# Kernel optimization log

Measured on AMD Instinct MI355X. Metric: run time of the kernel, lower is better.

The kernel has to match this reference:

```python
import jax, jax.numpy as jnp
import numpy as np

NUM_EMBEDDINGS = 1024
EMBEDDING_DIM = 256
COMMITMENT_COST = 0.25


def setup_inputs() -> dict:
    key = jax.random.key(0)
    k_z, k_e = jax.random.split(key)
    z = jax.random.normal(k_z, (16, EMBEDDING_DIM, 4096), dtype=jnp.float32)
    # nn.Embedding init: uniform(-1/K, 1/K)
    emb = jax.random.uniform(
        k_e, (NUM_EMBEDDINGS, EMBEDDING_DIM), dtype=jnp.float32,
        minval=-1.0 / NUM_EMBEDDINGS, maxval=1.0 / NUM_EMBEDDINGS)
    return {"z": z, "emb": emb}


def reference(z, emb):
    # z: [B, D, T] -> [B, T, D]
    zt = jnp.transpose(z, (0, 2, 1))
    B, T, D = zt.shape
    flat = zt.reshape(-1, D)  # [N, D]
    dists = (jnp.sum(flat * flat, axis=1, keepdims=True)
             + jnp.sum(emb * emb, axis=1)
             - 2.0 * jnp.matmul(flat, emb.T))
    idx = jnp.argmin(dists, axis=1)          # [N]
    quantized = emb[idx].reshape(B, T, D)    # gather + reshape
    e_latent_loss = jnp.mean((jax.lax.stop_gradient(quantized) - zt) ** 2)
    q_latent_loss = jnp.mean((quantized - jax.lax.stop_gradient(zt)) ** 2)
    loss = q_latent_loss + COMMITMENT_COST * e_latent_loss
    # straight-through estimator
    quantized_st = zt + jax.lax.stop_gradient(quantized - zt)
    return jnp.transpose(quantized_st, (0, 2, 1)), loss
```

## Files before the change

kernel.cpp:

```cpp
#include <hip/hip_runtime.h>
#include <stdint.h>

#define B_   16
#define D_   256
#define T_   4096
#define K_   1024
#define N_   (B_ * T_)
#define BM   64

typedef __attribute__((ext_vector_type(4))) float floatx4;
typedef __attribute__((ext_vector_type(2))) float floatx2;
typedef __attribute__((ext_vector_type(2))) long longx2;

__global__ __launch_bounds__(256) void emb_prep(const float* __restrict__ emb,
                                                uint32_t* __restrict__ embf8,
                                                float* __restrict__ esqh,
                                                float* __restrict__ lossp) {
    int w = threadIdx.x >> 6, lane = threadIdx.x & 63;
    int k = blockIdx.x * 4 + w;
    float4 v = ((const float4*)emb)[k * 64 + lane];
    float a0 = v.x * 1024.f, a1 = v.y * 1024.f, a2 = v.z * 1024.f, a3 = v.w * 1024.f;
    int p = __builtin_amdgcn_cvt_pk_fp8_f32(a0, a1, 0, false);
    p = __builtin_amdgcn_cvt_pk_fp8_f32(a2, a3, p, true);
    int kk = lane >> 3, quad = (lane >> 1) & 3;
    int widx = (k >> 4) * 1024 + (kk >> 1) * 256 + (quad * 16 + (k & 15)) * 4
             + (kk & 1) * 2 + (lane & 1);
    embf8[widx] = (uint32_t)p;
    float ss = a0 * a0 + a1 * a1 + a2 * a2 + a3 * a3;
    #pragma unroll
    for (int off = 32; off; off >>= 1) ss += __shfl_xor(ss, off, 64);
    if (lane == 0) esqh[k] = ss * (0.5f / 1024.f);
    if (blockIdx.x == 0 && threadIdx.x == 0) *lossp = 0.f;
}

__global__ __launch_bounds__(256, 4) void vq_main(const float* __restrict__ z,
                                                  const uint32_t* __restrict__ embf8,
                                                  const float* __restrict__ esqh,
                                                  float* __restrict__ out0,
                                                  float* __restrict__ lossp) {
    __shared__ __align__(16) unsigned char xs[BM * 256];
    __shared__ float wvals[4][BM];
    __shared__ int   pidx[BM];
    __shared__ float zred[4];

    int tid  = threadIdx.x;
    int lane = tid & 63, w = tid >> 6;
    int ml   = lane & 15, quad = lane >> 4;
    int ph   = w >> 1, ch = w & 1;
    int blk  = blockIdx.x;
    int b    = blk >> 6;
    int t0   = (blk & 63) * BM;
    const float* zb = z + (size_t)b * (D_ * T_) + t0;

    float zsq = 0.f;
    {
        int t = lane, hf = (t >> 4) & 1;
        #pragma unroll 2
        for (int j = 0; j < 8; ++j) {
            int dgrp = w + 4 * j;
            int d0 = dgrp * 8;
            float f0 = zb[(d0 + 0) * T_ + t];
            float f1 = zb[(d0 + 1) * T_ + t];
            float f2 = zb[(d0 + 2) * T_ + t];
            float f3 = zb[(d0 + 3) * T_ + t];
            float f4 = zb[(d0 + 4) * T_ + t];
            float f5 = zb[(d0 + 5) * T_ + t];
            float f6 = zb[(d0 + 6) * T_ + t];
            float f7 = zb[(d0 + 7) * T_ + t];
            zsq += f0*f0 + f1*f1 + f2*f2 + f3*f3 + f4*f4 + f5*f5 + f6*f6 + f7*f7;
            uint32_t p0 = (uint32_t)__builtin_amdgcn_cvt_pk_fp8_f32(-f0, -f1, 0, false);
            p0 = (uint32_t)__builtin_amdgcn_cvt_pk_fp8_f32(-f2, -f3, (int)p0, true);
            uint32_t p1 = (uint32_t)__builtin_amdgcn_cvt_pk_fp8_f32(-f4, -f5, 0, false);
            p1 = (uint32_t)__builtin_amdgcn_cvt_pk_fp8_f32(-f6, -f7, (int)p1, true);
            int c = dgrp >> 1, h = dgrp & 1;
            *(uint2*)&xs[t * 256 + ((c ^ (t & 15)) << 4) + ((h ^ hf) << 3)] =
                make_uint2(p0, p1);
        }
    }

    int ct0 = ch * 32;
    const char* ebL = (const char*)embf8 + (size_t)ct0 * 4096 + (size_t)lane * 16;
    longx2 qqA[4], qqB[4];
    float ehA, ehB;
    #pragma unroll
    for (int i = 0; i < 4; ++i)
        qqA[i] = *(const longx2*)(ebL + i * 1024);
    ehA = esqh[ct0 * 16 + ml];

    __syncthreads();

    long afr[2][8];
    #pragma unroll
    for (int ss = 0; ss < 2; ++ss) {
        int s = 2 * ph + ss;
        int pnt = s * 16 + ml;
        #pragma unroll
        for (int kk = 0; kk < 8; ++kk) {
            int c = 2 * kk + (quad >> 1), h = quad & 1;
            afr[ss][kk] = *(const long*)&xs[pnt * 256 + ((c ^ ml) << 4) + ((h ^ (s & 1)) << 3)];
        }
    }

    float bv[2][4];
    #pragma unroll
    for (int ss = 0; ss < 2; ++ss)
        #pragma unroll
        for (int i = 0; i < 4; ++i) bv[ss][i] = 1e30f;

    const floatx4 zv = {0.f, 0.f, 0.f, 0.f};
    const unsigned hi_mask = 0xFFFFFC00u;

#define VQ_PREFETCH(QQ, EH, J)                                                  \
    {                                                                           \
        const char* p_ = ebL + (size_t)(J) * 4096;                              \
        _Pragma("unroll")                                                       \
        for (int i = 0; i < 4; ++i)                                             \
            QQ[i] = *(const longx2*)(p_ + i * 1024);                            \
        EH = esqh[(ct0 + (J)) * 16 + ml];                                       \
    }

#define VQ_STEP(QQ, EH, J)                                                      \
    {                                                                           \
        floatx4 ehv = {EH, EH, EH, EH};                                         \
        floatx4 lo0, lo1, hi0, hi1;                                             \
        lo0 = __builtin_amdgcn_mfma_f32_16x16x32_fp8_fp8(afr[0][0], QQ[0][0], ehv, 0, 0, 0); \
        lo1 = __builtin_amdgcn_mfma_f32_16x16x32_fp8_fp8(afr[1][0], QQ[0][0], ehv, 0, 0, 0); \
        hi0 = __builtin_amdgcn_mfma_f32_16x16x32_fp8_fp8(afr[0][4], QQ[2][0], zv,  0, 0, 0); \
        hi1 = __builtin_amdgcn_mfma_f32_16x16x32_fp8_fp8(afr[1][4], QQ[2][0], zv,  0, 0, 0); \
        lo0 = __builtin_amdgcn_mfma_f32_16x16x32_fp8_fp8(afr[0][1], QQ[0][1], lo0, 0, 0, 0); \
        lo1 = __builtin_amdgcn_mfma_f32_16x16x32_fp8_fp8(afr[1][1], QQ[0][1], lo1, 0, 0, 0); \
        hi0 = __builtin_amdgcn_mfma_f32_16x16x32_fp8_fp8(afr[0][5], QQ[2][1], hi0, 0, 0, 0); \
        hi1 = __builtin_amdgcn_mfma_f32_16x16x32_fp8_fp8(afr[1][5], QQ[2][1], hi1, 0, 0, 0); \
        lo0 = __builtin_amdgcn_mfma_f32_16x16x32_fp8_fp8(afr[0][2], QQ[1][0], lo0, 0, 0, 0); \
        lo1 = __builtin_amdgcn_mfma_f32_16x16x32_fp8_fp8(afr[1][2], QQ[1][0], lo1, 0, 0, 0); \
        hi0 = __builtin_amdgcn_mfma_f32_16x16x32_fp8_fp8(afr[0][6], QQ[3][0], hi0, 0, 0, 0); \
        hi1 = __builtin_amdgcn_mfma_f32_16x16x32_fp8_fp8(afr[1][6], QQ[3][0], hi1, 0, 0, 0); \
        lo0 = __builtin_amdgcn_mfma_f32_16x16x32_fp8_fp8(afr[0][3], QQ[1][1], lo0, 0, 0, 0); \
        lo1 = __builtin_amdgcn_mfma_f32_16x16x32_fp8_fp8(afr[1][3], QQ[1][1], lo1, 0, 0, 0); \
        hi0 = __builtin_amdgcn_mfma_f32_16x16x32_fp8_fp8(afr[0][7], QQ[3][1], hi0, 0, 0, 0); \
        hi1 = __builtin_amdgcn_mfma_f32_16x16x32_fp8_fp8(afr[1][7], QQ[3][1], hi1, 0, 0, 0); \
        unsigned cbits = (unsigned)((ct0 + (J)) * 16 + ml);                     \
        _Pragma("unroll")                                                       \
        for (int i = 0; i < 4; ++i) {                                           \
            float d0 = lo0[i] + hi0[i];                                         \
            bv[0][i] = fminf(bv[0][i], __uint_as_float((__float_as_uint(d0) & hi_mask) | cbits)); \
            float d1 = lo1[i] + hi1[i];                                         \
            bv[1][i] = fminf(bv[1][i], __uint_as_float((__float_as_uint(d1) & hi_mask) | cbits)); \
        }                                                                       \
    }

    #pragma unroll 1
    for (int j = 0; j < 32; j += 2) {
        VQ_PREFETCH(qqB, ehB, j + 1)
        VQ_STEP(qqA, ehA, j)
        if (j + 2 < 32)
            VQ_PREFETCH(qqA, ehA, j + 2)
        VQ_STEP(qqB, ehB, j + 1)
    }

#undef VQ_PREFETCH
#undef VQ_STEP

    #pragma unroll
    for (int ss = 0; ss < 2; ++ss)
        #pragma unroll
        for (int i = 0; i < 4; ++i) {
            float v = bv[ss][i];
            #pragma unroll
            for (int off = 1; off < 16; off <<= 1)
                v = fminf(v, __shfl_xor(v, off, 64));
            if (ml == 0) wvals[w][(2 * ph + ss) * 16 + quad * 4 + i] = v;
        }
    #pragma unroll
    for (int off = 32; off; off >>= 1) zsq += __shfl_xor(zsq, off, 64);
    if (lane == 0) zred[w] = zsq;
    __syncthreads();

    if (tid < 64) {
        int t = tid, qb = (t >> 5) * 2;
        float wv = fminf(wvals[qb][t], wvals[qb + 1][t]);
        pidx[t] = (int)(__float_as_uint(wv) & 1023u);
        float lsum = wv;
        #pragma unroll
        for (int off = 32; off; off >>= 1) lsum += __shfl_xor(lsum, off, 64);
        if (t == 0) {
            float tot = zred[0] + zred[1] + zred[2] + zred[3] + lsum * (2.0f / 1024.f);
            atomicAdd(lossp, tot * (1.25f / 16777216.0f));
        }
    }
    __syncthreads();

    #pragma unroll
    for (int m = 0; m < 4; ++m) {
        int t = (tid >> 4) + 16 * m;
        int g = tid & 15;
        int code = pidx[t];
        const char* src = (const char*)embf8 + (size_t)(code >> 4) * 4096
                        + (g >> 2) * 1024 + ((g & 3) * 16 + (code & 15)) * 16;
        uint4 v = *(const uint4*)src;
        *(uint4*)&xs[t * 256 + ((g ^ (t & 15)) << 4)] = v;
    }
    __syncthreads();

    float* ob = out0 + (size_t)b * (D_ * T_) + t0;
    {
        int t = lane;
        #pragma unroll
        for (int jj = 0; jj < 4; ++jj) {
            int g = w + 4 * jj;
            uint4 v = *(const uint4*)&xs[t * 256 + ((g ^ (t & 15)) << 4)];
            uint32_t wd[4] = {v.x, v.y, v.z, v.w};
            #pragma unroll
            for (int u = 0; u < 4; ++u) {
                int kk = (g >> 2) * 2 + (u >> 1);
                int d0 = kk * 32 + (g & 3) * 8 + (u & 1) * 4;
                floatx2 lo = __builtin_amdgcn_cvt_pk_f32_fp8((int)wd[u], false);
                floatx2 hi = __builtin_amdgcn_cvt_pk_f32_fp8((int)wd[u], true);
                ob[(d0 + 0) * T_ + t] = lo[0] * (1.f / 1024.f);
                ob[(d0 + 1) * T_ + t] = lo[1] * (1.f / 1024.f);
                ob[(d0 + 2) * T_ + t] = hi[0] * (1.f / 1024.f);
                ob[(d0 + 3) * T_ + t] = hi[1] * (1.f / 1024.f);
            }
        }
    }
}

extern "C" void kernel_launch(void* const* d_in, const int* in_sizes, int n_in,
                              void* d_out, int out_size, void* d_ws, size_t ws_size,
                              hipStream_t stream) {
    (void)in_sizes; (void)n_in; (void)out_size; (void)ws_size;
    const float* z   = (const float*)d_in[0];
    const float* emb = (const float*)d_in[1];

    uint32_t* embf8 = (uint32_t*)d_ws;
    float*    esqh  = (float*)((char*)d_ws + (size_t)K_ * D_);

    float* out0  = (float*)d_out;
    float* lossp = out0 + (size_t)N_ * D_;

    emb_prep<<<K_ / 4, 256, 0, stream>>>(emb, embf8, esqh, lossp);
    vq_main<<<N_ / BM, 256, 0, stream>>>(z, embf8, esqh, out0, lossp);
}
```

Baseline: 133.2 us.

## Process two point tiles per block, overlapping z loads and output stores with MFMA

Each block now handles two 64-point tiles and interleaves stages across them. Tile B's z loads and fp8 conversion run inside tile A's distance loop. Tile A's codebook gather and output store are spread across tile B's MFMA loop. The goal is to hide global memory latency behind matrix compute. The cost is double shared memory, higher register pressure, occupancy lowered to 2 blocks per SIMD target, and half as many blocks in the grid.

```diff
diff --git a/kernel.cpp b/kernel.cpp
--- a/kernel.cpp
+++ b/kernel.cpp
@@ -33,12 +33,13 @@
     if (blockIdx.x == 0 && threadIdx.x == 0) *lossp = 0.f;
 }
 
-__global__ __launch_bounds__(256, 4) void vq_main(const float* __restrict__ z,
+__global__ __launch_bounds__(256, 2) void vq_main(const float* __restrict__ z,
                                                   const uint32_t* __restrict__ embf8,
                                                   const float* __restrict__ esqh,
                                                   float* __restrict__ out0,
                                                   float* __restrict__ lossp) {
-    __shared__ __align__(16) unsigned char xs[BM * 256];
+    __shared__ __align__(16) unsigned char xsA[BM * 256];
+    __shared__ __align__(16) unsigned char xsB[BM * 256];
     __shared__ float wvals[4][BM];
     __shared__ int   pidx[BM];
     __shared__ float zred[4];
@@ -48,65 +49,43 @@
     int ml   = lane & 15, quad = lane >> 4;
     int ph   = w >> 1, ch = w & 1;
     int blk  = blockIdx.x;
-    int b    = blk >> 6;
-    int t0   = (blk & 63) * BM;
-    const float* zb = z + (size_t)b * (D_ * T_) + t0;
-
-    float zsq = 0.f;
+    int b    = blk >> 5;
+    int t0   = (blk & 31) * (2 * BM);
+    const float* zbA = z + (size_t)b * (D_ * T_) + t0;
+    const float* zbB = zbA + BM;
+    float* obA = out0 + (size_t)b * (D_ * T_) + t0;
+    float* obB = obA + BM;
+
+    float zsqA = 0.f, zsqB = 0.f;
     {
         int t = lane, hf = (t >> 4) & 1;
         #pragma unroll 2
         for (int j = 0; j < 8; ++j) {
             int dgrp = w + 4 * j;
             int d0 = dgrp * 8;
-            float f0 = zb[(d0 + 0) * T_ + t];
-            float f1 = zb[(d0 + 1) * T_ + t];
-            float f2 = zb[(d0 + 2) * T_ + t];
-            float f3 = zb[(d0 + 3) * T_ + t];
-            float f4 = zb[(d0 + 4) * T_ + t];
-            float f5 = zb[(d0 + 5) * T_ + t];
-            float f6 = zb[(d0 + 6) * T_ + t];
-            float f7 = zb[(d0 + 7) * T_ + t];
-            zsq += f0*f0 + f1*f1 + f2*f2 + f3*f3 + f4*f4 + f5*f5 + f6*f6 + f7*f7;
+            float f0 = zbA[(d0 + 0) * T_ + t];
+            float f1 = zbA[(d0 + 1) * T_ + t];
+            float f2 = zbA[(d0 + 2) * T_ + t];
+            float f3 = zbA[(d0 + 3) * T_ + t];
+            float f4 = zbA[(d0 + 4) * T_ + t];
+            float f5 = zbA[(d0 + 5) * T_ + t];
+            float f6 = zbA[(d0 + 6) * T_ + t];
+            float f7 = zbA[(d0 + 7) * T_ + t];
+            zsqA += f0*f0 + f1*f1 + f2*f2 + f3*f3 + f4*f4 + f5*f5 + f6*f6 + f7*f7;
             uint32_t p0 = (uint32_t)__builtin_amdgcn_cvt_pk_fp8_f32(-f0, -f1, 0, false);
             p0 = (uint32_t)__builtin_amdgcn_cvt_pk_fp8_f32(-f2, -f3, (int)p0, true);
             uint32_t p1 = (uint32_t)__builtin_amdgcn_cvt_pk_fp8_f32(-f4, -f5, 0, false);
             p1 = (uint32_t)__builtin_amdgcn_cvt_pk_fp8_f32(-f6, -f7, (int)p1, true);
             int c = dgrp >> 1, h = dgrp & 1;
-            *(uint2*)&xs[t * 256 + ((c ^ (t & 15)) << 4) + ((h ^ hf) << 3)] =
+            *(uint2*)&xsA[t * 256 + ((c ^ (t & 15)) << 4) + ((h ^ hf) << 3)] =
                 make_uint2(p0, p1);
         }
     }
 
     int ct0 = ch * 32;
     const char* ebL = (const char*)embf8 + (size_t)ct0 * 4096 + (size_t)lane * 16;
-    longx2 qqA[4], qqB[4];
-    float ehA, ehB;
-    #pragma unroll
-    for (int i = 0; i < 4; ++i)
-        qqA[i] = *(const longx2*)(ebL + i * 1024);
-    ehA = esqh[ct0 * 16 + ml];
-
-    __syncthreads();
-
-    long afr[2][8];
-    #pragma unroll
-    for (int ss = 0; ss < 2; ++ss) {
-        int s = 2 * ph + ss;
-        int pnt = s * 16 + ml;
-        #pragma unroll
-        for (int kk = 0; kk < 8; ++kk) {
-            int c = 2 * kk + (quad >> 1), h = quad & 1;
-            afr[ss][kk] = *(const long*)&xs[pnt * 256 + ((c ^ ml) << 4) + ((h ^ (s & 1)) << 3)];
-        }
-    }
-
-    float bv[2][4];
-    #pragma unroll
-    for (int ss = 0; ss < 2; ++ss)
-        #pragma unroll
-        for (int i = 0; i < 4; ++i) bv[ss][i] = 1e30f;
-
+    longx2 qq0[4], qq1[4];
+    float eh0, eh1;
     const floatx4 zv = {0.f, 0.f, 0.f, 0.f};
     const unsigned hi_mask = 0xFFFFFC00u;
 
@@ -149,17 +128,65 @@
         }                                                                       \
     }
 
+#define VQ_K2(J)                                                                \
+    VQ_PREFETCH(qq1, eh1, (J) + 1)                                              \
+    VQ_STEP(qq0, eh0, (J))                                                      \
+    if ((J) + 2 < 32) VQ_PREFETCH(qq0, eh0, (J) + 2)                            \
+    VQ_STEP(qq1, eh1, (J) + 1)
+
+    VQ_PREFETCH(qq0, eh0, 0)
+    __syncthreads();
+
+    long afr[2][8];
+    #pragma unroll
+    for (int ss = 0; ss < 2; ++ss) {
+        int s = 2 * ph + ss;
+        int pnt = s * 16 + ml;
+        #pragma unroll
+        for (int kk = 0; kk < 8; ++kk) {
+            int c = 2 * kk + (quad >> 1), h = quad & 1;
+            afr[ss][kk] = *(const long*)&xsA[pnt * 256 + ((c ^ ml) << 4) + ((h ^ (s & 1)) << 3)];
+        }
+    }
+
+    float bv[2][4];
+    #pragma unroll
+    for (int ss = 0; ss < 2; ++ss)
+        #pragma unroll
+        for (int i = 0; i < 4; ++i) bv[ss][i] = 1e30f;
+
     #pragma unroll 1
-    for (int j = 0; j < 32; j += 2) {
-        VQ_PREFETCH(qqB, ehB, j + 1)
-        VQ_STEP(qqA, ehA, j)
-        if (j + 2 < 32)
-            VQ_PREFETCH(qqA, ehA, j + 2)
-        VQ_STEP(qqB, ehB, j + 1)
-    }
-
-#undef VQ_PREFETCH
-#undef VQ_STEP
+    for (int jj = 0; jj < 8; ++jj) {
+        int j = 4 * jj;
+        int t = lane, hf = (t >> 4) & 1;
+        int dgrp = w + 4 * jj, d0 = dgrp * 8;
+        VQ_PREFETCH(qq1, eh1, j + 1)
+        float f0 = zbB[(d0 + 0) * T_ + t];
+        float f1 = zbB[(d0 + 1) * T_ + t];
+        float f2 = zbB[(d0 + 2) * T_ + t];
+        float f3 = zbB[(d0 + 3) * T_ + t];
+        float f4 = zbB[(d0 + 4) * T_ + t];
+        float f5 = zbB[(d0 + 5) * T_ + t];
+        float f6 = zbB[(d0 + 6) * T_ + t];
+        float f7 = zbB[(d0 + 7) * T_ + t];
+        VQ_STEP(qq0, eh0, j)
+        VQ_PREFETCH(qq0, eh0, j + 2)
+        VQ_STEP(qq1, eh1, j + 1)
+        zsqB += f0*f0 + f1*f1 + f2*f2 + f3*f3 + f4*f4 + f5*f5 + f6*f6 + f7*f7;
+        {
+            uint32_t p0 = (uint32_t)__builtin_amdgcn_cvt_pk_fp8_f32(-f0, -f1, 0, false);
+            p0 = (uint32_t)__builtin_amdgcn_cvt_pk_fp8_f32(-f2, -f3, (int)p0, true);
+            uint32_t p1 = (uint32_t)__builtin_amdgcn_cvt_pk_fp8_f32(-f4, -f5, 0, false);
+            p1 = (uint32_t)__builtin_amdgcn_cvt_pk_fp8_f32(-f6, -f7, (int)p1, true);
+            int c = dgrp >> 1, h = dgrp & 1;
+            *(uint2*)&xsB[t * 256 + ((c ^ (t & 15)) << 4) + ((h ^ hf) << 3)] =
+                make_uint2(p0, p1);
+        }
+        VQ_PREFETCH(qq1, eh1, j + 3)
+        VQ_STEP(qq0, eh0, j + 2)
+        if (j + 4 < 32) VQ_PREFETCH(qq0, eh0, j + 4)
+        VQ_STEP(qq1, eh1, j + 3)
+    }
 
     #pragma unroll
     for (int ss = 0; ss < 2; ++ss)
@@ -172,8 +199,111 @@
             if (ml == 0) wvals[w][(2 * ph + ss) * 16 + quad * 4 + i] = v;
         }
     #pragma unroll
-    for (int off = 32; off; off >>= 1) zsq += __shfl_xor(zsq, off, 64);
-    if (lane == 0) zred[w] = zsq;
+    for (int off = 32; off; off >>= 1) zsqA += __shfl_xor(zsqA, off, 64);
+    if (lane == 0) zred[w] = zsqA;
+    __syncthreads();
+
+    if (tid < 64) {
+        int t = tid, qb = (t >> 5) * 2;
+        float wv = fminf(wvals[qb][t], wvals[qb + 1][t]);
+        pidx[t] = (int)(__float_as_uint(wv) & 1023u);
+        float lsum = wv;
+        #pragma unroll
+        for (int off = 32; off; off >>= 1) lsum += __shfl_xor(lsum, off, 64);
+        if (t == 0) {
+            float tot = zred[0] + zred[1] + zred[2] + zred[3] + lsum * (2.0f / 1024.f);
+            atomicAdd(lossp, tot * (1.25f / 16777216.0f));
+        }
+    }
+    __syncthreads();
+
+    #pragma unroll
+    for (int ss = 0; ss < 2; ++ss) {
+        int s = 2 * ph + ss;
+        int pnt = s * 16 + ml;
+        #pragma unroll
+        for (int kk = 0; kk < 8; ++kk) {
+            int c = 2 * kk + (quad >> 1), h = quad & 1;
+            afr[ss][kk] = *(const long*)&xsB[pnt * 256 + ((c ^ ml) << 4) + ((h ^ (s & 1)) << 3)];
+        }
+    }
+    #pragma unroll
+    for (int ss = 0; ss < 2; ++ss)
+        #pragma unroll
+        for (int i = 0; i < 4; ++i) bv[ss][i] = 1e30f;
+
+    VQ_PREFETCH(qq0, eh0, 0)
+
+    uint4 g0, g1, g2, g3;
+    {
+        int trow = tid >> 4, gcol = tid & 15;
+        int base = (gcol >> 2) * 1024 + (gcol & 3) * 16 * 16;
+        int c0 = pidx[trow +  0];
+        int c1 = pidx[trow + 16];
+        int c2 = pidx[trow + 32];
+        int c3 = pidx[trow + 48];
+        const char* eb = (const char*)embf8;
+        g0 = *(const uint4*)(eb + (size_t)(c0 >> 4) * 4096 + base + (c0 & 15) * 16);
+        g1 = *(const uint4*)(eb + (size_t)(c1 >> 4) * 4096 + base + (c1 & 15) * 16);
+        g2 = *(const uint4*)(eb + (size_t)(c2 >> 4) * 4096 + base + (c2 & 15) * 16);
+        g3 = *(const uint4*)(eb + (size_t)(c3 >> 4) * 4096 + base + (c3 & 15) * 16);
+    }
+
+    VQ_K2(0) VQ_K2(2) VQ_K2(4) VQ_K2(6)
+
+    {
+        int trow = tid >> 4, gcol = tid & 15;
+        int col = (gcol ^ trow) << 4;
+        *(uint4*)&xsA[(trow +  0) * 256 + col] = g0;
+        *(uint4*)&xsA[(trow + 16) * 256 + col] = g1;
+        *(uint4*)&xsA[(trow + 32) * 256 + col] = g2;
+        *(uint4*)&xsA[(trow + 48) * 256 + col] = g3;
+    }
+    __syncthreads();
+
+    VQ_K2(8) VQ_K2(10) VQ_K2(12) VQ_K2(14)
+
+    {
+        int t = lane;
+        #pragma unroll
+        for (int jj = 0; jj < 4; ++jj) {
+            int g = w + 4 * jj;
+            uint4 v = *(const uint4*)&xsA[t * 256 + ((g ^ (t & 15)) << 4)];
+            uint32_t wd[4] = {v.x, v.y, v.z, v.w};
+            #pragma unroll
+            for (int u = 0; u < 4; ++u) {
+                int kk = (g >> 2) * 2 + (u >> 1);
+                int d0 = kk * 32 + (g & 3) * 8 + (u & 1) * 4;
+                floatx2 lo = __builtin_amdgcn_cvt_pk_f32_fp8((int)wd[u], false);
+                floatx2 hi = __builtin_amdgcn_cvt_pk_f32_fp8((int)wd[u], true);
+                obA[(d0 + 0) * T_ + t] = lo[0] * (1.f / 1024.f);
+                obA[(d0 + 1) * T_ + t] = lo[1] * (1.f / 1024.f);
+                obA[(d0 + 2) * T_ + t] = hi[0] * (1.f / 1024.f);
+                obA[(d0 + 3) * T_ + t] = hi[1] * (1.f / 1024.f);
+            }
+        }
+    }
+
+    VQ_K2(16) VQ_K2(18) VQ_K2(20) VQ_K2(22)
+    VQ_K2(24) VQ_K2(26) VQ_K2(28) VQ_K2(30)
+
+#undef VQ_K2
+#undef VQ_PREFETCH
+#undef VQ_STEP
+
+    #pragma unroll
+    for (int ss = 0; ss < 2; ++ss)
+        #pragma unroll
+        for (int i = 0; i < 4; ++i) {
+            float v = bv[ss][i];
+            #pragma unroll
+            for (int off = 1; off < 16; off <<= 1)
+                v = fminf(v, __shfl_xor(v, off, 64));
+            if (ml == 0) wvals[w][(2 * ph + ss) * 16 + quad * 4 + i] = v;
+        }
+    #pragma unroll
+    for (int off = 32; off; off >>= 1) zsqB += __shfl_xor(zsqB, off, 64);
+    if (lane == 0) zred[w] = zsqB;
     __syncthreads();
 
     if (tid < 64) {
@@ -198,17 +328,16 @@
         const char* src = (const char*)embf8 + (size_t)(code >> 4) * 4096
                         + (g >> 2) * 1024 + ((g & 3) * 16 + (code & 15)) * 16;
         uint4 v = *(const uint4*)src;
-        *(uint4*)&xs[t * 256 + ((g ^ (t & 15)) << 4)] = v;
-    }
-    __syncthreads();
-
-    float* ob = out0 + (size_t)b * (D_ * T_) + t0;
+        *(uint4*)&xsB[t * 256 + ((g ^ (t & 15)) << 4)] = v;
+    }
+    __syncthreads();
+
     {
         int t = lane;
         #pragma unroll
         for (int jj = 0; jj < 4; ++jj) {
             int g = w + 4 * jj;
-            uint4 v = *(const uint4*)&xs[t * 256 + ((g ^ (t & 15)) << 4)];
+            uint4 v = *(const uint4*)&xsB[t * 256 + ((g ^ (t & 15)) << 4)];
             uint32_t wd[4] = {v.x, v.y, v.z, v.w};
             #pragma unroll
             for (int u = 0; u < 4; ++u) {
@@ -216,10 +345,10 @@
                 int d0 = kk * 32 + (g & 3) * 8 + (u & 1) * 4;
                 floatx2 lo = __builtin_amdgcn_cvt_pk_f32_fp8((int)wd[u], false);
                 floatx2 hi = __builtin_amdgcn_cvt_pk_f32_fp8((int)wd[u], true);
-                ob[(d0 + 0) * T_ + t] = lo[0] * (1.f / 1024.f);
-                ob[(d0 + 1) * T_ + t] = lo[1] * (1.f / 1024.f);
-                ob[(d0 + 2) * T_ + t] = hi[0] * (1.f / 1024.f);
-                ob[(d0 + 3) * T_ + t] = hi[1] * (1.f / 1024.f);
+                obB[(d0 + 0) * T_ + t] = lo[0] * (1.f / 1024.f);
+                obB[(d0 + 1) * T_ + t] = lo[1] * (1.f / 1024.f);
+                obB[(d0 + 2) * T_ + t] = hi[0] * (1.f / 1024.f);
+                obB[(d0 + 3) * T_ + t] = hi[1] * (1.f / 1024.f);
             }
         }
     }
@@ -239,5 +368,5 @@
     float* lossp = out0 + (size_t)N_ * D_;
 
     emb_prep<<<K_ / 4, 256, 0, stream>>>(emb, embf8, esqh, lossp);
-    vq_main<<<N_ / BM, 256, 0, stream>>>(z, embf8, esqh, out0, lossp);
+    vq_main<<<N_ / (2 * BM), 256, 0, stream>>>(z, embf8, esqh, out0, lossp);
 }
```

Measured after the change: 268.8 us. +101.9%, slower.
